# Optimization experiments

Hardware: AMD Instinct MI355X
Metric: run time of the kernel (lower is better)

Reference implementation:

```python
import jax, jax.numpy as jnp
import numpy as np

# my_conv from Sufficient-Vision-Transformer: unfold + per-channel weighted sums
# over k*k patch positions (two weight sets), concat, interleave channels, add bias.
# This is exactly a depthwise conv with 2 filters per input channel, output
# channels interleaved as [res1_0, res2_0, res1_1, res2_1, ...].

K = 3       # kernel_size
PAD = 1     # padding
STRIDE = 1  # stride


def setup_inputs() -> dict:
    key = jax.random.key(0)
    k1, k2, k3, k4 = jax.random.split(key, 4)
    B, C, H, W = 32, 192, 56, 56
    x = jax.random.normal(k1, (B, C, H, W), dtype=jnp.float32)
    weight1 = jax.random.normal(k2, (1, 1, C, K * K), dtype=jnp.float32)
    weight2 = jax.random.normal(k3, (1, 1, C, K * K), dtype=jnp.float32)
    bias = jax.random.normal(k4, (1, 2 * C, 1, 1), dtype=jnp.float32)
    return {"x": x, "weight1": weight1, "weight2": weight2, "bias": bias}


def reference(x, weight1, weight2, bias):
    B, C, H, W = x.shape
    # torch Unfold orders patch rows channel-major, kernel positions row-major
    # (kh, kw) -> matches reshape of weight (C, k*k) -> (C, 1, k, k).
    w1 = weight1.reshape(C, 1, K, K)
    w2 = weight2.reshape(C, 1, K, K)
    # Interleave filters per group: group i -> output channels [2i, 2i+1]
    # with feature_group_count=C; reproduces order_list = [0, C, 1, C+1, ...].
    w = jnp.stack([w1, w2], axis=1).reshape(2 * C, 1, K, K)
    out = jax.lax.conv_general_dilated(
        x, w,
        window_strides=(STRIDE, STRIDE),
        padding=[(PAD, PAD), (PAD, PAD)],
        feature_group_count=C,
        dimension_numbers=("NCHW", "OIHW", "NCHW"),
    )
    return out + bias
```

## Files before the change

### kernel.cpp

```cpp
#include <hip/hip_runtime.h>


#define BB 32
#define CC 192
#define HH 56
#define WW 56
#define W4 14
#define PITCH 60
#define LROWS 58

typedef float f32x4 __attribute__((ext_vector_type(4)));

__global__ __launch_bounds__(784) void dwconv2_lds_kernel(
    const float* __restrict__ x,
    const float* __restrict__ w1,
    const float* __restrict__ w2,
    const float* __restrict__ bias,
    float* __restrict__ out)
{
    __shared__ float tile[LROWS * PITCH];
    __shared__ float wts[20];

    const int bc = blockIdx.x;
    const int c  = bc % CC;

    const int t  = threadIdx.x;
    const int h  = t / W4;
    const int w4 = t % W4;
    const int w0 = w4 * 4;

    if (t < 9)        wts[t]      = w1[c * 9 + t];
    else if (t < 18)  wts[t]      = w2[c * 9 + (t - 9)];
    else if (t < 20)  wts[t]      = bias[2 * c + (t - 18)];

    if (t < 60)            tile[t] = 0.f;
    else if (t < 120)      tile[57 * PITCH + (t - 60)] = 0.f;
    else if (t < 176)      tile[(t - 119) * PITCH] = 0.f;
    else if (t < 232)      tile[(t - 175) * PITCH + 57] = 0.f;

    const f32x4 v = __builtin_nontemporal_load(
        (const f32x4*)(x + ((size_t)bc * HH + h) * WW + w0));
    float* dst = &tile[(h + 1) * PITCH + 1 + w0];
    dst[0] = v.x; dst[1] = v.y; dst[2] = v.z; dst[3] = v.w;

    __syncthreads();

    float a1[9], a2[9];
#pragma unroll
    for (int i = 0; i < 9; ++i) { a1[i] = wts[i]; a2[i] = wts[9 + i]; }
    const float bias1 = wts[18], bias2 = wts[19];

    float o1[4], o2[4];
#pragma unroll
    for (int p = 0; p < 4; ++p) { o1[p] = bias1; o2[p] = bias2; }

#pragma unroll
    for (int r = 0; r < 3; ++r) {
        const float* rp = &tile[(h + r) * PITCH + w0];
        float rv[6];
#pragma unroll
        for (int j = 0; j < 6; ++j) rv[j] = rp[j];
#pragma unroll
        for (int p = 0; p < 4; ++p) {
#pragma unroll
            for (int kc = 0; kc < 3; ++kc) {
                o1[p] += rv[p + kc] * a1[r * 3 + kc];
                o2[p] += rv[p + kc] * a2[r * 3 + kc];
            }
        }
    }

    const size_t obase = (((size_t)(bc * 2) * HH) + h) * WW + w0;
    f32x4 s1; s1.x = o1[0]; s1.y = o1[1]; s1.z = o1[2]; s1.w = o1[3];
    f32x4 s2; s2.x = o2[0]; s2.y = o2[1]; s2.z = o2[2]; s2.w = o2[3];
    __builtin_nontemporal_store(s1, (f32x4*)(out + obase));
    __builtin_nontemporal_store(s2, (f32x4*)(out + obase + (size_t)HH * WW));
}

extern "C" void kernel_launch(void* const* d_in, const int* in_sizes, int n_in,
                              void* d_out, int out_size, void* d_ws, size_t ws_size,
                              hipStream_t stream) {
    const float* x  = (const float*)d_in[0];
    const float* w1 = (const float*)d_in[1];
    const float* w2 = (const float*)d_in[2];
    const float* bs = (const float*)d_in[3];
    float* out = (float*)d_out;

    dwconv2_lds_kernel<<<BB * CC, 784, 0, stream>>>(x, w1, w2, bs, out);
}
```

Measured before the change: 238.7 us.

## Replace LDS tile with direct global loads and 4-row register tiling per thread

Drops the per-plane shared-memory tile and barrier. Each thread now reads its input rows straight from global memory (halo values come from scalar neighbour loads) and computes a 4x4 output tile for both filters, reusing each loaded row across up to three output rows. The grid changes to a flat launch of 256-thread blocks with an occupancy hint. This removes LDS traffic and synchronisation but adds redundant halo loads served from cache, plus more registers per thread.

```diff
diff --git a/kernel.cpp b/kernel.cpp
--- a/kernel.cpp
+++ b/kernel.cpp
@@ -6,75 +6,85 @@
 #define HH 56
 #define WW 56
 #define W4 14
-#define PITCH 60
-#define LROWS 58
+#define RT 4
+#define HQ (HH / RT)
+#define TPP (W4 * HQ)
+#define NSEG (BB * CC * TPP)
+#define TPB 256
 
 typedef float f32x4 __attribute__((ext_vector_type(4)));
 
-__global__ __launch_bounds__(784) void dwconv2_lds_kernel(
+__global__ __launch_bounds__(TPB, 6) void dwconv2_direct_kernel(
     const float* __restrict__ x,
     const float* __restrict__ w1,
     const float* __restrict__ w2,
     const float* __restrict__ bias,
     float* __restrict__ out)
 {
-    __shared__ float tile[LROWS * PITCH];
-    __shared__ float wts[20];
+    const int idx = blockIdx.x * TPB + threadIdx.x;
 
-    const int bc = blockIdx.x;
-    const int c  = bc % CC;
+    const int bc  = idx / TPP;
+    const int rem = idx % TPP;
+    const int hq  = rem / W4;
+    const int w4  = rem % W4;
+    const int h0  = hq * RT;
+    const int w0  = w4 * 4;
 
-    const int t  = threadIdx.x;
-    const int h  = t / W4;
-    const int w4 = t % W4;
-    const int w0 = w4 * 4;
-
-    if (t < 9)        wts[t]      = w1[c * 9 + t];
-    else if (t < 18)  wts[t]      = w2[c * 9 + (t - 9)];
-    else if (t < 20)  wts[t]      = bias[2 * c + (t - 18)];
-
-    if (t < 60)            tile[t] = 0.f;
-    else if (t < 120)      tile[57 * PITCH + (t - 60)] = 0.f;
-    else if (t < 176)      tile[(t - 119) * PITCH] = 0.f;
-    else if (t < 232)      tile[(t - 175) * PITCH + 57] = 0.f;
-
-    const f32x4 v = __builtin_nontemporal_load(
-        (const f32x4*)(x + ((size_t)bc * HH + h) * WW + w0));
-    float* dst = &tile[(h + 1) * PITCH + 1 + w0];
-    dst[0] = v.x; dst[1] = v.y; dst[2] = v.z; dst[3] = v.w;
-
-    __syncthreads();
+    const float* __restrict__ plane = x + (size_t)bc * (HH * WW);
+    const int c = bc % CC;
 
     float a1[9], a2[9];
 #pragma unroll
-    for (int i = 0; i < 9; ++i) { a1[i] = wts[i]; a2[i] = wts[9 + i]; }
-    const float bias1 = wts[18], bias2 = wts[19];
+    for (int i = 0; i < 9; ++i) { a1[i] = w1[c * 9 + i]; a2[i] = w2[c * 9 + i]; }
+    const float b1 = bias[2 * c], b2 = bias[2 * c + 1];
 
-    float o1[4], o2[4];
+    float o1[RT][4], o2[RT][4];
 #pragma unroll
-    for (int p = 0; p < 4; ++p) { o1[p] = bias1; o2[p] = bias2; }
+    for (int p = 0; p < RT; ++p)
+#pragma unroll
+        for (int j = 0; j < 4; ++j) { o1[p][j] = b1; o2[p][j] = b2; }
 
 #pragma unroll
-    for (int r = 0; r < 3; ++r) {
-        const float* rp = &tile[(h + r) * PITCH + w0];
+    for (int r = 0; r < RT + 2; ++r) {
+        const int ir = h0 - 1 + r;
         float rv[6];
+        if (ir >= 0 && ir < HH) {
+            const float* rp = plane + ir * WW + w0;
+            const f32x4 m = *(const f32x4*)rp;
+            rv[1] = m.x; rv[2] = m.y; rv[3] = m.z; rv[4] = m.w;
+            rv[0] = (w4 > 0)      ? rp[-1] : 0.f;
+            rv[5] = (w4 < W4 - 1) ? rp[4]  : 0.f;
+        } else {
 #pragma unroll
-        for (int j = 0; j < 6; ++j) rv[j] = rp[j];
+            for (int j = 0; j < 6; ++j) rv[j] = 0.f;
+        }
 #pragma unroll
-        for (int p = 0; p < 4; ++p) {
+        for (int p = 0; p < RT; ++p) {
+            if (p >= r - 2 && p <= r) {
+                const int k = r - p;
 #pragma unroll
-            for (int kc = 0; kc < 3; ++kc) {
-                o1[p] += rv[p + kc] * a1[r * 3 + kc];
-                o2[p] += rv[p + kc] * a2[r * 3 + kc];
+                for (int kc = 0; kc < 3; ++kc) {
+                    const float wv1 = a1[k * 3 + kc];
+                    const float wv2 = a2[k * 3 + kc];
+#pragma unroll
+                    for (int j = 0; j < 4; ++j) {
+                        o1[p][j] += rv[j + kc] * wv1;
+                        o2[p][j] += rv[j + kc] * wv2;
+                    }
+                }
             }
         }
     }
 
-    const size_t obase = (((size_t)(bc * 2) * HH) + h) * WW + w0;
-    f32x4 s1; s1.x = o1[0]; s1.y = o1[1]; s1.z = o1[2]; s1.w = o1[3];
-    f32x4 s2; s2.x = o2[0]; s2.y = o2[1]; s2.z = o2[2]; s2.w = o2[3];
-    __builtin_nontemporal_store(s1, (f32x4*)(out + obase));
-    __builtin_nontemporal_store(s2, (f32x4*)(out + obase + (size_t)HH * WW));
+    const size_t obase = (size_t)(bc * 2) * (HH * WW);
+#pragma unroll
+    for (int p = 0; p < RT; ++p) {
+        f32x4 s1; s1.x = o1[p][0]; s1.y = o1[p][1]; s1.z = o1[p][2]; s1.w = o1[p][3];
+        f32x4 s2; s2.x = o2[p][0]; s2.y = o2[p][1]; s2.z = o2[p][2]; s2.w = o2[p][3];
+        const size_t off = obase + (size_t)(h0 + p) * WW + w0;
+        __builtin_nontemporal_store(s1, (f32x4*)(out + off));
+        __builtin_nontemporal_store(s2, (f32x4*)(out + off + (size_t)(HH * WW)));
+    }
 }
 
 extern "C" void kernel_launch(void* const* d_in, const int* in_sizes, int n_in,
@@ -86,5 +96,5 @@
     const float* bs = (const float*)d_in[3];
     float* out = (float*)d_out;
 
-    dwconv2_lds_kernel<<<BB * CC, 784, 0, stream>>>(x, w1, w2, bs, out);
+    dwconv2_direct_kernel<<<NSEG / TPB, TPB, 0, stream>>>(x, w1, w2, bs, out);
 }
```

Result: slower. 263.8 us (+10.5%).

## Process several batch images per block with double-buffered LDS prefetch

Applied to the files above, without the earlier changes.

Each block now handles four batch images for the same channel, loading the weights and zeroing the halo once, instead of one image per block. LDS is double-buffered, and the global load for the next image is issued before the current image's convolution is computed, so memory latency overlaps with compute. This cuts the grid to a quarter of the blocks and amortises per-block setup. The trade-off is less parallelism from fewer blocks, twice the LDS per block, and a hand-placed barrier sequence.

```diff
diff --git a/kernel.cpp b/kernel.cpp
--- a/kernel.cpp
+++ b/kernel.cpp
@@ -8,40 +8,47 @@
 #define W4 14
 #define PITCH 60
 #define LROWS 58
+#define PPB 4
+#define NGRP (BB / PPB)
 
 typedef float f32x4 __attribute__((ext_vector_type(4)));
 
-__global__ __launch_bounds__(784) void dwconv2_lds_kernel(
+__global__ __launch_bounds__(784) void dwconv2_pipe_kernel(
     const float* __restrict__ x,
     const float* __restrict__ w1,
     const float* __restrict__ w2,
     const float* __restrict__ bias,
     float* __restrict__ out)
 {
-    __shared__ float tile[LROWS * PITCH];
+    __shared__ float tile[2][LROWS * PITCH];
     __shared__ float wts[20];
 
-    const int bc = blockIdx.x;
-    const int c  = bc % CC;
+    const int blk = blockIdx.x;
+    const int c   = blk % CC;
+    const int b0  = (blk / CC) * PPB;
 
     const int t  = threadIdx.x;
     const int h  = t / W4;
     const int w4 = t % W4;
     const int w0 = w4 * 4;
 
-    if (t < 9)        wts[t]      = w1[c * 9 + t];
-    else if (t < 18)  wts[t]      = w2[c * 9 + (t - 9)];
-    else if (t < 20)  wts[t]      = bias[2 * c + (t - 18)];
+    if (t < 9)        wts[t] = w1[c * 9 + t];
+    else if (t < 18)  wts[t] = w2[c * 9 + (t - 9)];
+    else if (t < 20)  wts[t] = bias[2 * c + (t - 18)];
 
-    if (t < 60)            tile[t] = 0.f;
-    else if (t < 120)      tile[57 * PITCH + (t - 60)] = 0.f;
-    else if (t < 176)      tile[(t - 119) * PITCH] = 0.f;
-    else if (t < 232)      tile[(t - 175) * PITCH + 57] = 0.f;
+#pragma unroll
+    for (int bf = 0; bf < 2; ++bf) {
+        if (t < 60)            tile[bf][t] = 0.f;
+        else if (t < 120)      tile[bf][57 * PITCH + (t - 60)] = 0.f;
+        else if (t < 176)      tile[bf][(t - 119) * PITCH] = 0.f;
+        else if (t < 232)      tile[bf][(t - 175) * PITCH + 57] = 0.f;
+    }
 
-    const f32x4 v = __builtin_nontemporal_load(
-        (const f32x4*)(x + ((size_t)bc * HH + h) * WW + w0));
-    float* dst = &tile[(h + 1) * PITCH + 1 + w0];
-    dst[0] = v.x; dst[1] = v.y; dst[2] = v.z; dst[3] = v.w;
+    const size_t hw = (size_t)HH * WW;
+    const int rowoff = h * WW + w0;
+
+    f32x4 v = __builtin_nontemporal_load(
+        (const f32x4*)(x + (size_t)(b0 * CC + c) * hw + rowoff));
 
     __syncthreads();
 
@@ -50,31 +57,48 @@
     for (int i = 0; i < 9; ++i) { a1[i] = wts[i]; a2[i] = wts[9 + i]; }
     const float bias1 = wts[18], bias2 = wts[19];
 
-    float o1[4], o2[4];
+    for (int i = 0; i < PPB; ++i) {
+        float* dst = &tile[i & 1][(h + 1) * PITCH + 1 + w0];
+        dst[0] = v.x; dst[1] = v.y; dst[2] = v.z; dst[3] = v.w;
+
+        if (i + 1 < PPB) {
+            v = __builtin_nontemporal_load(
+                (const f32x4*)(x + (size_t)((b0 + i + 1) * CC + c) * hw + rowoff));
+        }
+
+        asm volatile("s_waitcnt lgkmcnt(0)" ::: "memory");
+        __builtin_amdgcn_s_barrier();
+        __builtin_amdgcn_sched_barrier(0);
+        asm volatile("" ::: "memory");
+
+        float o1[4], o2[4];
 #pragma unroll
-    for (int p = 0; p < 4; ++p) { o1[p] = bias1; o2[p] = bias2; }
+        for (int p = 0; p < 4; ++p) { o1[p] = bias1; o2[p] = bias2; }
 
+        const float* tb = tile[i & 1];
 #pragma unroll
-    for (int r = 0; r < 3; ++r) {
-        const float* rp = &tile[(h + r) * PITCH + w0];
-        float rv[6];
+        for (int r = 0; r < 3; ++r) {
+            const float* rp = &tb[(h + r) * PITCH + w0];
+            float rv[6];
 #pragma unroll
-        for (int j = 0; j < 6; ++j) rv[j] = rp[j];
+            for (int j = 0; j < 6; ++j) rv[j] = rp[j];
 #pragma unroll
-        for (int p = 0; p < 4; ++p) {
+            for (int p = 0; p < 4; ++p) {
 #pragma unroll
-            for (int kc = 0; kc < 3; ++kc) {
-                o1[p] += rv[p + kc] * a1[r * 3 + kc];
-                o2[p] += rv[p + kc] * a2[r * 3 + kc];
+                for (int kc = 0; kc < 3; ++kc) {
+                    o1[p] += rv[p + kc] * a1[r * 3 + kc];
+                    o2[p] += rv[p + kc] * a2[r * 3 + kc];
+                }
             }
         }
+
+        const int bc = (b0 + i) * CC + c;
+        const size_t obase = ((size_t)(bc * 2) * HH + h) * WW + w0;
+        f32x4 s1; s1.x = o1[0]; s1.y = o1[1]; s1.z = o1[2]; s1.w = o1[3];
+        f32x4 s2; s2.x = o2[0]; s2.y = o2[1]; s2.z = o2[2]; s2.w = o2[3];
+        __builtin_nontemporal_store(s1, (f32x4*)(out + obase));
+        __builtin_nontemporal_store(s2, (f32x4*)(out + obase + hw));
     }
-
-    const size_t obase = (((size_t)(bc * 2) * HH) + h) * WW + w0;
-    f32x4 s1; s1.x = o1[0]; s1.y = o1[1]; s1.z = o1[2]; s1.w = o1[3];
-    f32x4 s2; s2.x = o2[0]; s2.y = o2[1]; s2.z = o2[2]; s2.w = o2[3];
-    __builtin_nontemporal_store(s1, (f32x4*)(out + obase));
-    __builtin_nontemporal_store(s2, (f32x4*)(out + obase + (size_t)HH * WW));
 }
 
 extern "C" void kernel_launch(void* const* d_in, const int* in_sizes, int n_in,
@@ -86,5 +110,5 @@
     const float* bs = (const float*)d_in[3];
     float* out = (float*)d_out;
 
-    dwconv2_lds_kernel<<<BB * CC, 784, 0, stream>>>(x, w1, w2, bs, out);
+    dwconv2_pipe_kernel<<<CC * NGRP, 784, 0, stream>>>(x, w1, w2, bs, out);
 }
```

Measured after the change: 216.3 us. 9.4% less time.
